# Optimization experiments

Hardware: AMD Instinct MI355X
Metric: run time of the kernel (lower is better)

Reference implementation:

```python
import jax, jax.numpy as jnp
import numpy as np

HEADS = 16
DIM_HEAD = 64


def shift(x):
    # Transformer-XL relative shift trick. x: [..., i, j] -> [..., i, j]
    *lead, i, j = x.shape
    x = jnp.concatenate([x, jnp.zeros((*lead, i, i), x.dtype)], axis=-1)
    l = i + j - 1
    x = x.reshape(*lead, -1)
    pad = (-x.shape[-1]) % l
    x = jnp.concatenate([x, jnp.zeros((*lead, pad), x.dtype)], axis=-1)
    x = x.reshape(*lead, -1, l)
    return x[..., :i, i - 1:]


def setup_inputs() -> dict:
    key = jax.random.key(0)
    ks = jax.random.split(key, 6)
    b, t, d = 4, 1024, 1024
    mem_len = 1024
    s = 0.02
    return {
        "x": jax.random.normal(ks[0], (b, t, d), jnp.float32),
        "mem": jax.random.normal(ks[1], (b, mem_len, d), jnp.float32),
        "wq": jax.random.normal(ks[2], (d, d), jnp.float32) * s,
        "wkv": jax.random.normal(ks[3], (d, 2 * d), jnp.float32) * s,
        "wo": jax.random.normal(ks[4], (d, d), jnp.float32) * s,
        "bo": jnp.zeros((d,), jnp.float32),
        "rel_w": jax.random.normal(ks[5], (t + mem_len, HEADS, DIM_HEAD), jnp.float32) * s,
    }


def reference(x, mem, wq, wkv, wo, bo, rel_w):
    b, t, d = x.shape
    h, dh = HEADS, DIM_HEAD
    mem_len = mem.shape[1]
    scale = dh ** -0.5

    q = x @ wq                                  # [b,t,d]
    kv_in = jnp.concatenate([mem, x], axis=1)   # [b,t+mem,d]
    k, v = jnp.split(kv_in @ wkv, 2, axis=-1)

    to_heads = lambda z: z.reshape(b, -1, h, dh).transpose(0, 2, 1, 3)
    q, k, v = to_heads(q), to_heads(k), to_heads(v)  # [b,h,*,dh]

    dots = jnp.einsum('bhid,bhjd->bhij', q, k) * scale      # [b,h,t,t+mem]
    w = rel_w[: t + mem_len]                                 # [t+mem,h,dh]
    pos = shift(jnp.einsum('bhid,jhd->bhij', q, w) * scale)  # [b,h,t,t+mem]
    dots = dots + pos

    jdim = t + mem_len
    mask = jnp.triu(jnp.ones((t, jdim), bool), k=1 + mem_len)
    dots = jnp.where(mask[None, None], -jnp.inf, dots)
    attn = jax.nn.softmax(dots, axis=-1)

    out = jnp.einsum('bhij,bhjd->bhid', attn, v)
    out = out.transpose(0, 2, 1, 3).reshape(b, t, d)
    out = out @ wo + bo

    mem_next = jnp.concatenate([mem, x], axis=1)[:, -mem_len:]  # t == seq_len branch
    return out, mem_next
```

## Files before the change

### kernel.cpp

```cpp
#include <hip/hip_runtime.h>
#include <cstddef>
#include <cstdint>

#define B_DIM 4
#define T_DIM 1024
#define D_DIM 1024
#define H_DIM 16
#define DH 64
#define JDIM 2048
#define MEMLEN 1024
#define RELPAD 2176

typedef float floatx4 __attribute__((ext_vector_type(4)));
typedef short short8 __attribute__((ext_vector_type(8)));

static __device__ __forceinline__ short f2bf(float f) {
    union { float f; uint32_t u; } v; v.f = f;
    uint32_t r = (v.u + 0x7FFFu + ((v.u >> 16) & 1u)) >> 16;
    return (short)r;
}

static __device__ __forceinline__ void gl_lds16(const short* g, short* l) {
    __builtin_amdgcn_global_load_lds(
        (const __attribute__((address_space(1))) void*)g,
        (__attribute__((address_space(3))) void*)l, 16, 0, 0);
}

template <int CTRL>
static __device__ __forceinline__ float dpp_fmax(float v) {
    int y = __builtin_amdgcn_update_dpp(0, __builtin_bit_cast(int, v),
                                        CTRL, 0xF, 0xF, true);
    return fmaxf(v, __builtin_bit_cast(float, y));
}
static __device__ __forceinline__ float row16_max(float v) {
    v = dpp_fmax<0xB1>(v);
    v = dpp_fmax<0x4E>(v);
    v = dpp_fmax<0x124>(v);
    v = dpp_fmax<0x128>(v);
    return v;
}

__global__ __launch_bounds__(256) void prep_all(
    const float* __restrict__ x, const float* __restrict__ mem,
    const float* __restrict__ rel,
    float* __restrict__ mem_next, short* __restrict__ kvb,
    const float* __restrict__ wq, const float* __restrict__ wkv,
    const float* __restrict__ wo, short* __restrict__ wkvqT,
    short* __restrict__ woT, short* __restrict__ relb) {
    __shared__ float tile[32][33];
    const int bx = blockIdx.x;
    const int tid = threadIdx.x;

    if (bx < 8192) {
        const size_t gid = (size_t)bx * 256 + tid;
        if (gid < 1048576) {
            const size_t idx = gid * 4;
            float4 v = *(const float4*)(x + idx);
            *(float4*)(mem_next + idx) = v;
            const int b = (int)(idx >> 20);
            const size_t r = idx & 1048575;
            short4 o;
            o.x = f2bf(v.x); o.y = f2bf(v.y); o.z = f2bf(v.z); o.w = f2bf(v.w);
            *(short4*)(kvb + (size_t)b * 2097152 + 1048576 + r) = o;
        } else {
            const size_t idx = (gid - 1048576) * 4;
            float4 v = *(const float4*)(mem + idx);
            const int b = (int)(idx >> 20);
            const size_t r = idx & 1048575;
            short4 o;
            o.x = f2bf(v.x); o.y = f2bf(v.y); o.z = f2bf(v.z); o.w = f2bf(v.w);
            *(short4*)(kvb + (size_t)b * 2097152 + r) = o;
        }
    } else if (bx < 14336) {
        const int i = bx - 8192;
        const int z = i >> 11;
        const int rem = i & 2047;
        const int gx = rem & 31, gy = rem >> 5;
        const int N = (z == 1) ? 2048 : 1024;
        if (gy * 32 >= N) return;
        const float* w = (z == 0) ? wq : (z == 1) ? wkv : wo;
        short* wT = (z == 0) ? (wkvqT + (size_t)2048 * 1024) : (z == 1) ? wkvqT : woT;
        const int k0 = gx * 32, n0 = gy * 32;
        const int tx = tid & 31, ty = tid >> 5;
        for (int r = ty; r < 32; r += 8)
            tile[r][tx] = w[(size_t)(k0 + r) * N + n0 + tx];
        __syncthreads();
        for (int r = ty; r < 32; r += 8)
            wT[(size_t)(n0 + r) * 1024 + k0 + tx] = f2bf(tile[tx][r]);
    } else {
        const int i = bx - 14336;
        const int gx = i % 136, gy = i / 136;
        const int h = gy;
        const int jp = gx * 16 + (tid >> 4);
        const int c = (tid & 15) << 2;
        float4 v = make_float4(0.f, 0.f, 0.f, 0.f);
        if (jp < JDIM) v = *(const float4*)(rel + ((size_t)jp * H_DIM + h) * DH + c);
        short4 o;
        o.x = f2bf(v.x); o.y = f2bf(v.y); o.z = f2bf(v.z); o.w = f2bf(v.w);
        *(short4*)(relb + ((size_t)h * RELPAD + jp) * DH + c) = o;
    }
}

template <int CMODE>
__global__ __launch_bounds__(256) void mfma_gemm(
    const short* __restrict__ A, const short* __restrict__ Bt,
    const float* __restrict__ bias,
    short* __restrict__ C0, short* __restrict__ C1, short* __restrict__ C2,
    float* __restrict__ Cf) {
    constexpr int K = 1024;
    constexpr int NT = K / 32;
    int bx = blockIdx.x, by = blockIdx.y;
    if (CMODE == 1) {
        const int L = by * 24 + bx;
        const int xcd = L & 7, m = L >> 3;
        by = ((m & 7) << 3) | xcd;
        bx = m >> 3;
    }
    const int row0 = by << 7, col0 = bx << 7;
    if (CMODE == 1 && col0 >= 2048 && (row0 & 2047) < 1024) return;

    __shared__ short ash[2][128 * 32];
    __shared__ short bsh[2][128 * 32];

    const int tid = threadIdx.x;
    const int w = tid >> 6, lane = tid & 63;
    const int l15 = lane & 15, quad = lane >> 4;
    const int wr = w >> 1, wc = w & 1;

    const int sk = (lane & 3) << 3;
    const short* ap0 = A + (size_t)(row0 + (w << 5) + (lane >> 2)) * K + sk;
    const short* ap1 = ap0 + (size_t)16 * K;
    const short* bp0 = Bt + (size_t)(col0 + (w << 5) + (lane >> 2)) * K + sk;
    const short* bp1 = bp0 + (size_t)16 * K;

    gl_lds16(ap0, ash[0] + (w << 10));
    gl_lds16(ap1, ash[0] + (w << 10) + 512);
    gl_lds16(bp0, bsh[0] + (w << 10));
    gl_lds16(bp1, bsh[0] + (w << 10) + 512);
    __syncthreads();

    floatx4 acc[4][4] = {};

#pragma unroll 2
    for (int t = 0; t < NT; ++t) {
        const int cur = t & 1;
        if (t + 1 < NT) {
            const int nxt = cur ^ 1;
            const int k1 = (t + 1) << 5;
            gl_lds16(ap0 + k1, ash[nxt] + (w << 10));
            gl_lds16(ap1 + k1, ash[nxt] + (w << 10) + 512);
            gl_lds16(bp0 + k1, bsh[nxt] + (w << 10));
            gl_lds16(bp1 + k1, bsh[nxt] + (w << 10) + 512);
        }

        short8 af[4];
#pragma unroll
        for (int mt = 0; mt < 4; ++mt)
            af[mt] = *(const short8*)&ash[cur][(((wr << 6) + (mt << 4) + l15) << 5) + (quad << 3)];
#pragma unroll
        for (int nt = 0; nt < 4; ++nt) {
            short8 bf = *(const short8*)&bsh[cur][(((wc << 6) + (nt << 4) + l15) << 5) + (quad << 3)];
#pragma unroll
            for (int mt = 0; mt < 4; ++mt)
                acc[mt][nt] = __builtin_amdgcn_mfma_f32_16x16x32_bf16(af[mt], bf, acc[mt][nt], 0, 0, 0);
        }
        __syncthreads();
    }

#pragma unroll
    for (int nt = 0; nt < 4; ++nt) {
        const int col = col0 + (wc << 6) + (nt << 4) + l15;
        float bv = (CMODE == 2) ? bias[col] : 0.f;
#pragma unroll
        for (int mt = 0; mt < 4; ++mt) {
#pragma unroll
            for (int rr = 0; rr < 4; ++rr) {
                const int row = row0 + (wr << 6) + (mt << 4) + (quad << 2) + rr;
                const float val = acc[mt][nt][rr];
                if (CMODE == 1) {
                    int b = row >> 11, j = row & 2047;
                    if (col < 1024) {
                        int h = col >> 6, c = col & 63;
                        C0[(((size_t)b * H_DIM + h) * JDIM + j) * DH + c] = f2bf(val);
                    } else if (col < 2048) {
                        int n2 = col - 1024, h = n2 >> 6, c = n2 & 63;
                        C1[(((size_t)b * H_DIM + h) * DH + c) * JDIM + j] = f2bf(val);
                    } else {
                        int n2 = col - 2048, h = n2 >> 6, c = n2 & 63;
                        int i = j - 1024;
                        C2[(((size_t)b * H_DIM + h) * T_DIM + i) * DH + c] =
                            f2bf(val * 0.18033688f);
                    }
                } else {
                    Cf[(size_t)row * 1024 + col] = val + bv;
                }
            }
        }
    }
}

__global__ __launch_bounds__(256, 4) void flash_attn(
    const short* __restrict__ qb, const short* __restrict__ kb,
    const short* __restrict__ vTb, const short* __restrict__ relb,
    short* __restrict__ ob) {
    __shared__ short kshf[8 * 512];
    __shared__ short vshf[8 * 512];
    __shared__ short rshf[3 * 8 * 512];

    const int tid = threadIdx.x;
    const int w = tid >> 6;
    const int lane = tid & 63;
    const int l15 = lane & 15, quad = lane >> 4;
    const int L = blockIdx.y * 16 + blockIdx.x;
    const int xcd = L & 7, m = L >> 3;
    const int bh = ((m & 7) << 3) | xcd;
    const int itile = m >> 3;
    const int h = bh & 15, b = bh >> 4;
    const int i0 = itile << 6;
    const int goff = 3 - w;

    const short* kb_b = kb + (size_t)bh * JDIM * DH;
    const short* vT_b = vTb + (size_t)bh * DH * JDIM;
    const short* rel_b = relb + (size_t)h * RELPAD * DH;

    const short* qrow = qb + ((size_t)bh * T_DIM + i0 + (w << 4) + l15) * DH;
    const short8 a_q0 = *(const short8*)(qrow + (quad << 3));
    const short8 a_q1 = *(const short8*)(qrow + 32 + (quad << 3));

    const int kc0 = w, kc1 = w + 4;
    const short* kp0 = kb_b + (size_t)(((kc0 >> 1) << 4) + l15) * DH + (kc0 & 1) * 32 + (quad << 3);
    const short* kp1 = kb_b + (size_t)(((kc1 >> 1) << 4) + l15) * DH + (kc1 & 1) * 32 + (quad << 3);
    const short* vp0 = vT_b + (size_t)(((kc0 >> 1) << 4) + l15) * JDIM + (kc0 & 1) * 32 + (quad << 3);
    const short* vp1 = vT_b + (size_t)(((kc1 >> 1) << 4) + l15) * JDIM + (kc1 & 1) * 32 + (quad << 3);
    const int base00 = 960 - i0;

    gl_lds16(kp0, kshf + (kc0 << 9));
    gl_lds16(kp1, kshf + (kc1 << 9));
    gl_lds16(vp0, vshf + (kc0 << 9));
    gl_lds16(vp1, vshf + (kc1 << 9));
    kp0 += 64 * DH; kp1 += 64 * DH; vp0 += 64; vp1 += 64;
#pragma unroll
    for (int s = 0; s < 4; ++s) {
        const int c4 = w + (s << 2);
        const short* rp = rel_b + (size_t)(base00 + ((c4 >> 1) << 4) + l15) * DH +
                          (c4 & 1) * 32 + (quad << 3);
        gl_lds16(rp, rshf + (c4 << 9));
    }
    const short* rw0 = rel_b + (size_t)(base00 + 128 + ((w >> 1) << 4) + l15) * DH +
                       (w & 1) * 32 + (quad << 3);
    const short* rw1 = rel_b + (size_t)(base00 + 128 + (((w + 4) >> 1) << 4) + l15) * DH +
                       ((w + 4) & 1) * 32 + (quad << 3);
    __syncthreads();

    short8 ones8;
#pragma unroll
    for (int z = 0; z < 8; ++z) ones8[z] = (short)0x3F80;

    int srcl[4];
    uint32_t psel[4];
#pragma unroll
    for (int r = 0; r < 4; ++r) {
        const int t = l15 - (quad << 2) - r + 15;
        psel[r] = (t >> 4) ? 0x01000404u : 0x03020404u;
        srcl[r] = (quad << 4) | (t & 15);
    }

    floatx4 o_acc[4] = {};
    float m_r[4], l_r[4];
#pragma unroll
    for (int r = 0; r < 4; ++r) { m_r[r] = -3.0e38f; l_r[r] = 0.f; }

    const int jt_end = itile + 17;
    int s0 = 0, s1 = 1, s2 = 2;

    for (int jt = 0; jt < jt_end; ++jt) {
        __builtin_amdgcn_s_setprio(1);
        floatx4 s_acc[4];
#pragma unroll
        for (int nt = 0; nt < 4; ++nt) {
            short8 bk0 = *(const short8*)&kshf[((nt << 1) << 9) + (lane << 3)];
            short8 bk1 = *(const short8*)&kshf[(((nt << 1) + 1) << 9) + (lane << 3)];
            floatx4 acc = {0.f, 0.f, 0.f, 0.f};
            acc = __builtin_amdgcn_mfma_f32_16x16x32_bf16(a_q0, bk0, acc, 0, 0, 0);
            acc = __builtin_amdgcn_mfma_f32_16x16x32_bf16(a_q1, bk1, acc, 0, 0, 0);
            s_acc[nt] = acc;
        }

        floatx4 G[5];
#pragma unroll
        for (int gi = 0; gi < 5; ++gi) {
            const int rb = gi + goff;
            const int seg = (rb & 4) ? s1 : s0;
            const int ch = (seg << 3) + ((rb & 3) << 1);
            short8 br0 = *(const short8*)&rshf[(ch << 9) + (lane << 3)];
            short8 br1 = *(const short8*)&rshf[((ch + 1) << 9) + (lane << 3)];
            floatx4 acc = {0.f, 0.f, 0.f, 0.f};
            acc = __builtin_amdgcn_mfma_f32_16x16x32_bf16(a_q0, br0, acc, 0, 0, 0);
            G[gi] = __builtin_amdgcn_mfma_f32_16x16x32_bf16(a_q1, br1, acc, 0, 0, 0);
        }
        __builtin_amdgcn_s_setprio(0);

        uint32_t pk[4][4];
#pragma unroll
        for (int gi = 0; gi < 4; ++gi)
#pragma unroll
            for (int r = 0; r < 4; ++r)
                pk[gi][r] = __builtin_amdgcn_perm(
                    __builtin_bit_cast(uint32_t, G[gi][r]),
                    __builtin_bit_cast(uint32_t, G[gi + 1][r]), 0x07060302u);
#pragma unroll
        for (int nt = 0; nt < 4; ++nt)
#pragma unroll
            for (int r = 0; r < 4; ++r) {
                uint32_t pv = (uint32_t)__shfl((int)pk[nt][r], srcl[r], 64);
                uint32_t gb = __builtin_amdgcn_perm(0u, pv, psel[r]);
                s_acc[nt][r] = s_acc[nt][r] + __builtin_bit_cast(float, gb);
            }
        if (jt == jt_end - 1) {
#pragma unroll
            for (int nt = 0; nt < 4; ++nt) {
                const int u = (nt << 4) + l15;
#pragma unroll
                for (int r = 0; r < 4; ++r) {
                    const int v = (w << 4) + (quad << 2) + r;
                    if (u > v) s_acc[nt][r] = -3.0e38f;
                }
            }
        }

        __syncthreads();
        if (jt + 1 < jt_end) {
            gl_lds16(kp0, kshf + (kc0 << 9));
            gl_lds16(kp1, kshf + (kc1 << 9));
            gl_lds16(rw0, rshf + (s2 << 12) + (w << 9));
            gl_lds16(rw1, rshf + (s2 << 12) + ((w + 4) << 9));
            kp0 += 64 * DH; kp1 += 64 * DH; rw0 += 64 * DH; rw1 += 64 * DH;
        }

        short* pshp = rshf + (s0 << 12);

        float tm[4];
        bool need = false;
#pragma unroll
        for (int r = 0; r < 4; ++r) {
            tm[r] = fmaxf(fmaxf(s_acc[0][r], s_acc[1][r]),
                          fmaxf(s_acc[2][r], s_acc[3][r]));
            need |= (tm[r] > m_r[r] + 8.0f);
        }
        if (__any((int)need)) {
#pragma unroll
            for (int r = 0; r < 4; ++r) {
                const float t = row16_max(tm[r]);
                const float mx = fmaxf(m_r[r], t);
                const float alpha = __builtin_amdgcn_exp2f(m_r[r] - mx);
                m_r[r] = mx;
                l_r[r] *= alpha;
#pragma unroll
                for (int ct = 0; ct < 4; ++ct) o_acc[ct][r] *= alpha;
            }
        }
#pragma unroll
        for (int r = 0; r < 4; ++r) {
            const int prow = (w << 4) + (quad << 2) + r;
            char* rowb = (char*)pshp + (prow << 7);
            const int swz = (prow & 7) << 4;
#pragma unroll
            for (int nt = 0; nt < 4; ++nt) {
                const float p = __builtin_amdgcn_exp2f(s_acc[nt][r] - m_r[r]);
                *(short*)(rowb + ((((nt << 5) + (l15 << 1))) ^ swz)) = f2bf(p);
            }
        }

        const int arow = (w << 4) + l15;
        const char* arowb = (const char*)pshp + (arow << 7);
        const int asw = (l15 & 7) << 4;
        const short8 a_p0 = *(const short8*)(arowb + ((quad << 4) ^ asw));
        const short8 a_p1 = *(const short8*)(arowb + ((64 + (quad << 4)) ^ asw));
        __builtin_amdgcn_s_setprio(1);
        floatx4 ls = {0.f, 0.f, 0.f, 0.f};
        ls = __builtin_amdgcn_mfma_f32_16x16x32_bf16(a_p0, ones8, ls, 0, 0, 0);
        ls = __builtin_amdgcn_mfma_f32_16x16x32_bf16(a_p1, ones8, ls, 0, 0, 0);
#pragma unroll
        for (int r = 0; r < 4; ++r) l_r[r] += ls[r];
#pragma unroll
        for (int ct = 0; ct < 4; ++ct) {
            short8 bv0 = *(const short8*)&vshf[((ct << 1) << 9) + (lane << 3)];
            short8 bv1 = *(const short8*)&vshf[(((ct << 1) + 1) << 9) + (lane << 3)];
            o_acc[ct] = __builtin_amdgcn_mfma_f32_16x16x32_bf16(a_p0, bv0, o_acc[ct], 0, 0, 0);
            o_acc[ct] = __builtin_amdgcn_mfma_f32_16x16x32_bf16(a_p1, bv1, o_acc[ct], 0, 0, 0);
        }
        __builtin_amdgcn_s_setprio(0);

        __syncthreads();
        if (jt + 1 < jt_end) {
            gl_lds16(vp0, vshf + (kc0 << 9));
            gl_lds16(vp1, vshf + (kc1 << 9));
            vp0 += 64; vp1 += 64;
        }
        const int t = s0; s0 = s1; s1 = s2; s2 = t;
    }

#pragma unroll
    for (int ct = 0; ct < 4; ++ct) {
#pragma unroll
        for (int r = 0; r < 4; ++r) {
            const int i = i0 + (w << 4) + (quad << 2) + r;
            const float val = o_acc[ct][r] / l_r[r];
            ob[((size_t)b * T_DIM + i) * D_DIM + h * DH + (ct << 4) + l15] = f2bf(val);
        }
    }
}

extern "C" void kernel_launch(void* const* d_in, const int* in_sizes, int n_in,
                              void* d_out, int out_size, void* d_ws, size_t ws_size,
                              hipStream_t stream) {
    const float* x = (const float*)d_in[0];
    const float* mem = (const float*)d_in[1];
    const float* wq = (const float*)d_in[2];
    const float* wkv = (const float*)d_in[3];
    const float* wo = (const float*)d_in[4];
    const float* bo = (const float*)d_in[5];
    const float* rel_w = (const float*)d_in[6];

    float* out = (float*)d_out;
    float* mem_next = out + (size_t)B_DIM * T_DIM * D_DIM;

    short* kvb = (short*)d_ws;
    short* qb = kvb + 8388608;
    short* kb = qb + 4194304;
    short* vTb = kb + 8388608;
    short* relb = vTb + 8388608;
    short* ob = relb + 2228224;
    short* wkvqT = ob + 4194304;
    short* woT = wkvqT + 3145728;

    hipLaunchKernelGGL(prep_all, dim3(16512), dim3(256), 0, stream,
                       x, mem, rel_w, mem_next, kvb, wq, wkv, wo,
                       wkvqT, woT, relb);

    hipLaunchKernelGGL((mfma_gemm<1>), dim3(24, 64), dim3(256), 0, stream,
                       kvb, wkvqT, nullptr, kb, vTb, qb, nullptr);

    hipLaunchKernelGGL(flash_attn, dim3(16, 64), dim3(256), 0, stream,
                       qb, kb, vTb, relb, ob);

    hipLaunchKernelGGL((mfma_gemm<2>), dim3(8, 32), dim3(256), 0, stream,
                       ob, woT, bo, nullptr, nullptr, nullptr, out);
}
```

Before: 312.7 us.

## Load relative-position tiles directly from global into registers instead of LDS ring

Drops the three-stage shared-memory ring for the relative-position weights. Each wave now reads its five 16-row rel tiles straight from global memory into registers every iteration, and a single dedicated P buffer takes the place of the rotating segment. This cuts LDS footprint, which could raise occupancy, and removes LDS write/read traffic and segment bookkeeping. In exchange the global loads are exposed at the start of each iteration with no prefetch, and rows overlapping between waves are fetched redundantly through cache.

```diff
diff --git a/kernel.cpp b/kernel.cpp
--- a/kernel.cpp
+++ b/kernel.cpp
@@ -205,7 +205,7 @@
     short* __restrict__ ob) {
     __shared__ short kshf[8 * 512];
     __shared__ short vshf[8 * 512];
-    __shared__ short rshf[3 * 8 * 512];
+    __shared__ short psh[8 * 512];
 
     const int tid = threadIdx.x;
     const int w = tid >> 6;
@@ -234,22 +234,13 @@
     const short* vp1 = vT_b + (size_t)(((kc1 >> 1) << 4) + l15) * JDIM + (kc1 & 1) * 32 + (quad << 3);
     const int base00 = 960 - i0;
 
+    const short* relp = rel_b + (size_t)(base00 + (goff << 4) + l15) * DH + (quad << 3);
+
     gl_lds16(kp0, kshf + (kc0 << 9));
     gl_lds16(kp1, kshf + (kc1 << 9));
     gl_lds16(vp0, vshf + (kc0 << 9));
     gl_lds16(vp1, vshf + (kc1 << 9));
     kp0 += 64 * DH; kp1 += 64 * DH; vp0 += 64; vp1 += 64;
-#pragma unroll
-    for (int s = 0; s < 4; ++s) {
-        const int c4 = w + (s << 2);
-        const short* rp = rel_b + (size_t)(base00 + ((c4 >> 1) << 4) + l15) * DH +
-                          (c4 & 1) * 32 + (quad << 3);
-        gl_lds16(rp, rshf + (c4 << 9));
-    }
-    const short* rw0 = rel_b + (size_t)(base00 + 128 + ((w >> 1) << 4) + l15) * DH +
-                       (w & 1) * 32 + (quad << 3);
-    const short* rw1 = rel_b + (size_t)(base00 + 128 + (((w + 4) >> 1) << 4) + l15) * DH +
-                       ((w + 4) & 1) * 32 + (quad << 3);
     __syncthreads();
 
     short8 ones8;
@@ -271,9 +262,16 @@
     for (int r = 0; r < 4; ++r) { m_r[r] = -3.0e38f; l_r[r] = 0.f; }
 
     const int jt_end = itile + 17;
-    int s0 = 0, s1 = 1, s2 = 2;
 
     for (int jt = 0; jt < jt_end; ++jt) {
+        short8 brr[5][2];
+#pragma unroll
+        for (int gi = 0; gi < 5; ++gi) {
+            brr[gi][0] = *(const short8*)(relp + gi * 1024);
+            brr[gi][1] = *(const short8*)(relp + gi * 1024 + 32);
+        }
+        relp += 4096;
+
         __builtin_amdgcn_s_setprio(1);
         floatx4 s_acc[4];
 #pragma unroll
@@ -289,14 +287,9 @@
         floatx4 G[5];
 #pragma unroll
         for (int gi = 0; gi < 5; ++gi) {
-            const int rb = gi + goff;
-            const int seg = (rb & 4) ? s1 : s0;
-            const int ch = (seg << 3) + ((rb & 3) << 1);
-            short8 br0 = *(const short8*)&rshf[(ch << 9) + (lane << 3)];
-            short8 br1 = *(const short8*)&rshf[((ch + 1) << 9) + (lane << 3)];
             floatx4 acc = {0.f, 0.f, 0.f, 0.f};
-            acc = __builtin_amdgcn_mfma_f32_16x16x32_bf16(a_q0, br0, acc, 0, 0, 0);
-            G[gi] = __builtin_amdgcn_mfma_f32_16x16x32_bf16(a_q1, br1, acc, 0, 0, 0);
+            acc = __builtin_amdgcn_mfma_f32_16x16x32_bf16(a_q0, brr[gi][0], acc, 0, 0, 0);
+            G[gi] = __builtin_amdgcn_mfma_f32_16x16x32_bf16(a_q1, brr[gi][1], acc, 0, 0, 0);
         }
         __builtin_amdgcn_s_setprio(0);
 
@@ -332,12 +325,8 @@
         if (jt + 1 < jt_end) {
             gl_lds16(kp0, kshf + (kc0 << 9));
             gl_lds16(kp1, kshf + (kc1 << 9));
-            gl_lds16(rw0, rshf + (s2 << 12) + (w << 9));
-            gl_lds16(rw1, rshf + (s2 << 12) + ((w + 4) << 9));
-            kp0 += 64 * DH; kp1 += 64 * DH; rw0 += 64 * DH; rw1 += 64 * DH;
-        }
-
-        short* pshp = rshf + (s0 << 12);
+            kp0 += 64 * DH; kp1 += 64 * DH;
+        }
 
         float tm[4];
         bool need = false;
@@ -362,7 +351,7 @@
 #pragma unroll
         for (int r = 0; r < 4; ++r) {
             const int prow = (w << 4) + (quad << 2) + r;
-            char* rowb = (char*)pshp + (prow << 7);
+            char* rowb = (char*)psh + (prow << 7);
             const int swz = (prow & 7) << 4;
 #pragma unroll
             for (int nt = 0; nt < 4; ++nt) {
@@ -372,7 +361,7 @@
         }
 
         const int arow = (w << 4) + l15;
-        const char* arowb = (const char*)pshp + (arow << 7);
+        const char* arowb = (const char*)psh + (arow << 7);
         const int asw = (l15 & 7) << 4;
         const short8 a_p0 = *(const short8*)(arowb + ((quad << 4) ^ asw));
         const short8 a_p1 = *(const short8*)(arowb + ((64 + (quad << 4)) ^ asw));
@@ -397,7 +386,6 @@
             gl_lds16(vp1, vshf + (kc1 << 9));
             vp0 += 64; vp1 += 64;
         }
-        const int t = s0; s0 = s1; s1 = s2; s2 = t;
     }
 
 #pragma unroll
```

Result: slower. 407.4 us (+30.3%).
